# Performance work log

Hardware: AMD Instinct MI355X
Metric: run time of the kernel (lower is better)

## Reference

```python
import jax, jax.numpy as jnp
import numpy as np

K_HARD = 32
K_RAND = 32
SCALE_MAX = 100.0
NEG_FILL = -10000.0
EPS = 1e-12


def _normalize(x):
    return x / jnp.maximum(jnp.linalg.norm(x, axis=1, keepdims=True), EPS)


def _dir_loss(sim, scale, key):
    # One direction of InfoNCE with hard topk negatives + random negatives.
    B = sim.shape[0]
    diag = jnp.eye(B, dtype=bool)
    pos = jnp.diagonal(sim)                       # [B] positives
    sim_neg = jnp.where(diag, NEG_FILL, sim)      # mask self-similarity
    # hard negatives: per-row topk over masked sims (hard_ratio = 1.0)
    hard_vals, hard_idx = jax.lax.top_k(sim_neg, K_HARD)
    # valid pool for random negatives: not diagonal, not already a hard neg
    valid = (~diag).at[jnp.arange(B)[:, None], hard_idx].set(False)
    # uniform sampling without replacement via random-score top_k (fully on-device,
    # replaces the per-row nonzero/randperm loop); B-1-K_HARD >> min_valid_negs here
    r = jnp.where(valid, jax.random.uniform(key, (B, B)), -1.0)
    _, pick = jax.lax.top_k(r, K_RAND)
    rand_vals = jnp.take_along_axis(sim, pick, axis=1)  # picks exclude diag -> sim == sim_neg
    # logits: [pos | hard | rand], target class 0, scaled cross-entropy
    logits = jnp.concatenate([pos[:, None], hard_vals, rand_vals], axis=1) * scale
    return -jnp.mean(jax.nn.log_softmax(logits, axis=1)[:, 0])


def reference(h_img, h_txt, logit_scale):
    a = _normalize(h_img)
    b = _normalize(h_txt)
    sim = a @ b.T                                 # [B, B]
    scale = jnp.minimum(jnp.exp(logit_scale[0]), SCALE_MAX)
    k1, k2 = jax.random.split(jax.random.key(42))
    loss_i2t = _dir_loss(sim, scale, k1)
    loss_t2i = _dir_loss(sim.T, scale, k2)
    return 0.5 * (loss_i2t + loss_t2i)


def setup_inputs() -> dict:
    key = jax.random.key(0)
    k1, k2 = jax.random.split(key)
    B, D = 8192, 1024
    h_img = jax.random.normal(k1, (B, D), dtype=jnp.float32)
    h_txt = jax.random.normal(k2, (B, D), dtype=jnp.float32)
    logit_scale = jnp.full((1,), np.log(1.0 / 0.07), dtype=jnp.float32)
    return {"h_img": h_img, "h_txt": h_txt, "logit_scale": logit_scale}
```

## Files before the change

### kernel.cpp

```cpp
#include <hip/hip_runtime.h>
#include <hip/hip_bf16.h>


#define BN8 8192
#define DK 1024
#define KH 32
#define KR 32
#define LDSZ 131072
#define NCB 128

typedef __attribute__((ext_vector_type(4))) float f32x4;
typedef __attribute__((ext_vector_type(8))) int i32x8;
typedef __attribute__((ext_vector_type(4))) int i32x4;

#if __has_builtin(__builtin_amdgcn_exp2f)
#define EXP2(x) __builtin_amdgcn_exp2f(x)
#else
#define EXP2(x) exp2f(x)
#endif

static __device__ __forceinline__ unsigned short f2bf(float f) {
  unsigned u = __float_as_uint(f);
  u = u + 0x7FFFu + ((u >> 16) & 1u);
  return (unsigned short)(u >> 16);
}
static __device__ __forceinline__ float bf2f(unsigned short v) {
  return __uint_as_float(((unsigned)v) << 16);
}
static __device__ __forceinline__ float keyval(unsigned u) {
  unsigned short v = (u & 0x8000u) ? (unsigned short)(u ^ 0x8000u) : (unsigned short)(~u);
  return bf2f(v);
}

static __device__ __forceinline__ unsigned pk_skey(unsigned w) {
  const unsigned m = ((w >> 15) & 0x00010001u) * 0x7FFFu;
  return w ^ (m | 0x80008000u);
}
static __device__ __forceinline__ unsigned pkmax(unsigned a, unsigned b) {
  unsigned d; asm("v_pk_max_u16 %0, %1, %2" : "=v"(d) : "v"(a), "v"(b)); return d;
}
static __device__ __forceinline__ unsigned pkmin(unsigned a, unsigned b) {
  unsigned d; asm("v_pk_min_u16 %0, %1, %2" : "=v"(d) : "v"(a), "v"(b)); return d;
}
#define INS4P(K0, K1, K2, K3, U) do { unsigned _u = (U); \
    unsigned _n0 = pkmin(K0, _u); K0 = pkmax(K0, _u); \
    unsigned _n1 = pkmin(K1, _n0); K1 = pkmax(K1, _n0); \
    unsigned _n2 = pkmin(K2, _n1); K2 = pkmax(K2, _n1); \
    K3 = pkmax(K3, _n2); } while (0)

__global__ __launch_bounds__(256) void norm_convert8(const float* __restrict__ img,
                                                     const float* __restrict__ txt,
                                                     unsigned char* __restrict__ a8,
                                                     unsigned char* __restrict__ b8) {
  const int row = blockIdx.x;
  const int t = threadIdx.x;
  const float* src;
  unsigned char* dst;
  if (row < BN8) { src = img + (size_t)row * DK; dst = a8 + (size_t)row * DK; }
  else          { src = txt + (size_t)(row - BN8) * DK; dst = b8 + (size_t)(row - BN8) * DK; }
  float4 v = ((const float4*)src)[t];
  float ss = v.x * v.x + v.y * v.y + v.z * v.z + v.w * v.w;
  for (int off = 32; off; off >>= 1) ss += __shfl_xor(ss, off);
  __shared__ float red[4];
  if ((t & 63) == 0) red[t >> 6] = ss;
  __syncthreads();
  float tot = red[0] + red[1] + red[2] + red[3];
  float inv = 1.0f / fmaxf(sqrtf(tot), 1e-12f);
  const int p0 = __builtin_amdgcn_cvt_pk_fp8_f32(v.x * inv, v.y * inv, 0, false);
  const int p1 = __builtin_amdgcn_cvt_pk_fp8_f32(v.z * inv, v.w * inv, 0, false);
  ((unsigned*)dst)[t] = ((unsigned)p0 & 0xFFFFu) | ((unsigned)p1 << 16);
}

#define GLDS(SRC, DST) __builtin_amdgcn_global_load_lds( \
    (const __attribute__((address_space(1))) void*)(SRC), \
    (__attribute__((address_space(3))) void*)(DST), 16, 0, 0)

template <int N> static __device__ __forceinline__ void vmwait() {
  if constexpr (N == 0) asm volatile("s_waitcnt vmcnt(0)" ::: "memory");
  else if constexpr (N == 1) asm volatile("s_waitcnt vmcnt(1)" ::: "memory");
  else if constexpr (N == 2) asm volatile("s_waitcnt vmcnt(2)" ::: "memory");
  else if constexpr (N == 3) asm volatile("s_waitcnt vmcnt(3)" ::: "memory");
  else if constexpr (N == 4) asm volatile("s_waitcnt vmcnt(4)" ::: "memory");
  else if constexpr (N == 5) asm volatile("s_waitcnt vmcnt(5)" ::: "memory");
  else if constexpr (N == 6) asm volatile("s_waitcnt vmcnt(6)" ::: "memory");
}

static __device__ __forceinline__ i32x8 pack8(const char* p0, const char* p1) {
  i32x4 lo = *(const i32x4*)p0;
  i32x4 hi = *(const i32x4*)p1;
  i32x8 r;
  r[0] = lo[0]; r[1] = lo[1]; r[2] = lo[2]; r[3] = lo[3];
  r[4] = hi[0]; r[5] = hi[1]; r[6] = hi[2]; r[7] = hi[3];
  return r;
}

template <int VM, bool STG, int MQ>
static __device__ __forceinline__ void phase8(const char* stg_src, int stg_lds,
                                              char* lds, int cur_off, int kbyte,
                                              int abyte, int bbyte, int sw0, int sw1,
                                              i32x8 (&bfr)[4], f32x4 (&acc)[8][4]) {
  vmwait<VM>();
  asm volatile("s_barrier" ::: "memory");
  const char* cb = lds + cur_off;
  i32x8 af[2];
#pragma unroll
  for (int j = 0; j < 2; ++j)
    af[j] = pack8(cb + abyte + (MQ * 2 + j) * 2048 + sw0,
                  cb + abyte + (MQ * 2 + j) * 2048 + sw1);
  if constexpr (MQ == 0) {
#pragma unroll
    for (int n = 0; n < 4; ++n)
      bfr[n] = pack8(cb + bbyte + n * 2048 + sw0, cb + bbyte + n * 2048 + sw1);
  }
  if constexpr (STG) {
    GLDS(stg_src + kbyte, lds + stg_lds);
    GLDS(stg_src + kbyte + 32768, lds + stg_lds + 4096);
  }
  __builtin_amdgcn_s_setprio(1);
#pragma unroll
  for (int j = 0; j < 2; ++j)
#pragma unroll
    for (int n = 0; n < 4; ++n)
      acc[MQ * 2 + j][n] = __builtin_amdgcn_mfma_scale_f32_16x16x128_f8f6f4(
          af[j], bfr[n], acc[MQ * 2 + j][n], 0, 0,
          0, 0x7F7F7F7F, 0, 0x7F7F7F7F);
  __builtin_amdgcn_s_setprio(0);
}

__global__ __launch_bounds__(512, 2) void gemm_fp8(const unsigned char* __restrict__ A,
                                                   const unsigned char* __restrict__ Bm,
                                                   unsigned short* __restrict__ C) {
  extern __shared__ char lds[];
  const int t = threadIdx.x;
  const int lane = t & 63;
  const int w = t >> 6;
  const int wr = w >> 2, wc = w & 3;
  const int wch = wc >> 1, g4 = wr * 2 + (wc & 1);
  const int llo = lane & 15, lhi = lane >> 4;

  const int bid = blockIdx.y * 32 + blockIdx.x;
  const int swz = (bid & 7) * 128 + (bid >> 3);
  const int row0 = (swz >> 5) << 8;
  const int col0 = (swz & 31) << 8;

  const int scol = (((lane & 7) ^ (lane >> 3)) << 4);
  const char* asg = (const char*)A +
      (size_t)(row0 + wr * 128 + wc * 8 + (lane >> 3)) * 1024 + scol;
  const char* bsg = (const char*)Bm +
      (size_t)(col0 + wch * 128 + g4 * 8 + (lane >> 3)) * 1024 + scol;
  const int ldsAo = wr * 16384 + wc * 1024;
  const int ldsBo = 32768 + wch * 16384 + g4 * 1024;

  const int sw0 = (((2 * lhi) ^ (llo & 7)) << 4);
  const int sw1 = sw0 ^ 16;
  const int abyte = wr * 16384 + llo * 128;
  const int bbyte = 32768 + wc * 8192 + llo * 128;

  f32x4 acc[8][4] = {};
  i32x8 bfr[4];

  {
#pragma unroll
    for (int e = 0; e < 4; ++e) GLDS(bsg + e * 32768, lds + ldsBo + e * 4096);
#pragma unroll
    for (int e = 0; e < 4; ++e) GLDS(asg + e * 32768, lds + ldsAo + e * 4096);
    asm volatile("s_waitcnt vmcnt(0)" ::: "memory");
    asm volatile("s_barrier" ::: "memory");
  }

  for (int u = 0; u < 7; ++u) {
    const int cur = (u & 1) << 16;
    const int nxt = cur ^ 65536;
    const int kb = (u + 1) * 128;
    phase8<3, true, 0>(bsg,         nxt + ldsBo,        lds, cur, kb, abyte, bbyte, sw0, sw1, bfr, acc);
    phase8<4, true, 1>(bsg + 65536, nxt + ldsBo + 8192, lds, cur, kb, abyte, bbyte, sw0, sw1, bfr, acc);
    phase8<5, true, 2>(asg,         nxt + ldsAo,        lds, cur, kb, abyte, bbyte, sw0, sw1, bfr, acc);
    phase8<6, true, 3>(asg + 65536, nxt + ldsAo + 8192, lds, cur, kb, abyte, bbyte, sw0, sw1, bfr, acc);
  }
  {
    const int cur = (7 & 1) << 16;
    phase8<3, false, 0>(asg, 0, lds, cur, 0, abyte, bbyte, sw0, sw1, bfr, acc);
    phase8<2, false, 1>(asg, 0, lds, cur, 0, abyte, bbyte, sw0, sw1, bfr, acc);
    phase8<1, false, 2>(asg, 0, lds, cur, 0, abyte, bbyte, sw0, sw1, bfr, acc);
    phase8<0, false, 3>(asg, 0, lds, cur, 0, abyte, bbyte, sw0, sw1, bfr, acc);
  }

  const int gr0 = row0 + wr * 128 + lhi * 4;
  const int gc0 = col0 + wc * 64 + llo;
#pragma unroll
  for (int m = 0; m < 8; ++m)
#pragma unroll
    for (int n = 0; n < 4; ++n) {
      const int gr = gr0 + m * 16;
      const int gc = gc0 + n * 16;
#pragma unroll
      for (int r = 0; r < 4; ++r)
        C[(size_t)(gr + r) * BN8 + gc] = f2bf(acc[m][n][r]);
    }
}

__global__ __launch_bounds__(512) void fused_reduce(const unsigned short* __restrict__ sim,
                                                    const float* __restrict__ lsc,
                                                    float* __restrict__ losses) {
  __shared__ float sW[8][64];
  __shared__ float hW[8][64];
  __shared__ unsigned mW[8][64];
  __shared__ float posL[64];
  __shared__ unsigned TL[64];
  __shared__ int cnt[18][64];

  const int t = threadIdx.x;
  const int lane = t & 63, w = t >> 6;
  const float s = fminf(__expf(lsc[0]), 100.0f);
  const float s2 = s * 1.44269504f;
  const float c2 = -s2;

  if (blockIdx.x >= NCB) {
    const int i = (blockIdx.x - NCB) * 8 + w;
    const uint4* rowp = (const uint4*)(sim + (size_t)i * BN8);
    uint4 ld[16];
#pragma unroll
    for (int k = 0; k < 16; ++k) ld[k] = rowp[lane + 64 * k];

    const int dlane = (i >> 3) & 63;
    const int dk = i >> 9;
    float pos = 0.f;
    if (lane == dlane) {
      const int wsel = (i >> 1) & 3;
#pragma unroll
      for (int k = 0; k < 16; ++k)
        if (k == dk) {
          unsigned w0;
          if (wsel == 0) w0 = ld[k].x; else if (wsel == 1) w0 = ld[k].y;
          else if (wsel == 2) w0 = ld[k].z; else w0 = ld[k].w;
          pos = bf2f((i & 1) ? (unsigned short)(w0 >> 16) : (unsigned short)(w0 & 0xFFFFu));
          const unsigned nw = (i & 1) ? ((w0 & 0x0000FFFFu) | 0xFF800000u)
                                      : ((w0 & 0xFFFF0000u) | 0x0000FF80u);
          if (wsel == 0) ld[k].x = nw; else if (wsel == 1) ld[k].y = nw;
          else if (wsel == 2) ld[k].z = nw; else ld[k].w = nw;
        }
    }
    pos = __shfl(pos, dlane);

    unsigned k0 = 0, k1 = 0, k2 = 0, k3 = 0;
    float esA = 0.f, esB = 0.f;
#define PWP(W) do { unsigned _w = (W); \
    INS4P(k0, k1, k2, k3, pk_skey(_w)); \
    esA += EXP2(fmaf(__uint_as_float(_w << 16), s2, c2)); \
    esB += EXP2(fmaf(__uint_as_float(_w & 0xFFFF0000u), s2, c2)); } while (0)
#pragma unroll
    for (int k = 0; k < 16; ++k) { PWP(ld[k].x); PWP(ld[k].y); PWP(ld[k].z); PWP(ld[k].w); }
    float es = esA + esB;

    unsigned mk;
    { unsigned a = k0 & 0xFFFFu, b = k0 >> 16; mk = a > b ? a : b; }
    for (int off = 32; off; off >>= 1) { unsigned o = __shfl_xor(mk, off); mk = o > mk ? o : mk; }

#define CNT8(MID) ((int)((k0 & 0xFFFFu) > (MID)) + (int)((k0 >> 16) > (MID)) + \
                   (int)((k1 & 0xFFFFu) > (MID)) + (int)((k1 >> 16) > (MID)) + \
                   (int)((k2 & 0xFFFFu) > (MID)) + (int)((k2 >> 16) > (MID)) + \
                   (int)((k3 & 0xFFFFu) > (MID)) + (int)((k3 >> 16) > (MID)))

    unsigned lo = mk > 576u ? mk - 576u : 0u, hi = mk;
    {
      int c = CNT8(lo);
      for (int off = 32; off; off >>= 1) c += __shfl_xor(c, off);
      if (c < KH) lo = 0;
    }
    while (lo < hi) {
      const unsigned mid = (lo + hi) >> 1;
      int c = CNT8(mid);
      for (int off = 32; off; off >>= 1) c += __shfl_xor(c, off);
      if (c <= KH - 1) hi = mid; else lo = mid + 1;
    }
    const unsigned T = lo;
    int cab = CNT8(T);
    for (int off = 32; off; off >>= 1) cab += __shfl_xor(cab, off);

    float hs = 0.f;
#define HCAND(KK) do { unsigned _a = (KK) & 0xFFFFu, _b = (KK) >> 16; \
    if (_a > T) hs += EXP2(fmaf(keyval(_a), s2, c2)); \
    if (_b > T) hs += EXP2(fmaf(keyval(_b), s2, c2)); } while (0)
    HCAND(k0); HCAND(k1); HCAND(k2); HCAND(k3);
    for (int off = 32; off; off >>= 1) { es += __shfl_xor(es, off); hs += __shfl_xor(hs, off); }

    if (lane == 0) {
      const float hard = hs + (float)(KH - cab) * EXP2(fmaf(keyval(T), s2, c2));
      const float valid = fmaxf(es - hard, 0.f);
      const float rho = (float)KR / (float)(BN8 - 1 - KH);
      const float D = EXP2(fmaf(pos, s2, c2)) + hard + rho * valid;
      losses[i] = s + __logf(D) - s * pos;
    }
    return;
  }

  const int q = t & 7, seg = t >> 3;
  const int c0b = blockIdx.x * 64;

  for (int j = t; j < 18 * 64; j += 512) ((int*)cnt)[j] = 0;

  unsigned kqp[4][4];
  float es[8];
#pragma unroll
  for (int c = 0; c < 4; ++c) {
    es[c * 2] = 0.f; es[c * 2 + 1] = 0.f;
#pragma unroll
    for (int r = 0; r < 4; ++r) kqp[c][r] = 0u;
  }

  const int cq = c0b + q * 8;
  const unsigned short* base = sim + (size_t)(seg * 128) * BN8 + cq;
  for (int rr = 0; rr < 128; rr += 4) {
    uint4 V0 = *(const uint4*)(base + (size_t)(rr + 0) * BN8);
    uint4 V1 = *(const uint4*)(base + (size_t)(rr + 1) * BN8);
    uint4 V2 = *(const uint4*)(base + (size_t)(rr + 2) * BN8);
    uint4 V3 = *(const uint4*)(base + (size_t)(rr + 3) * BN8);
#define COLROW(V, J) do { \
    const unsigned dd = (unsigned)(seg * 128 + rr + (J) - cq); \
    if (dd < 8u) { \
      const int wsel = dd >> 1; \
      unsigned w0; \
      if (wsel == 0) w0 = (V).x; else if (wsel == 1) w0 = (V).y; \
      else if (wsel == 2) w0 = (V).z; else w0 = (V).w; \
      posL[q * 8 + dd] = bf2f((dd & 1) ? (unsigned short)(w0 >> 16) \
                                       : (unsigned short)(w0 & 0xFFFFu)); \
      const unsigned nw = (dd & 1) ? ((w0 & 0x0000FFFFu) | 0xFF800000u) \
                                   : ((w0 & 0xFFFF0000u) | 0x0000FF80u); \
      if (wsel == 0) (V).x = nw; else if (wsel == 1) (V).y = nw; \
      else if (wsel == 2) (V).z = nw; else (V).w = nw; \
    } \
    const unsigned wd0 = (V).x, wd1 = (V).y, wd2 = (V).z, wd3 = (V).w; \
    INS4P(kqp[0][0], kqp[0][1], kqp[0][2], kqp[0][3], pk_skey(wd0)); \
    es[0] += EXP2(fmaf(__uint_as_float(wd0 << 16), s2, c2)); \
    es[1] += EXP2(fmaf(__uint_as_float(wd0 & 0xFFFF0000u), s2, c2)); \
    INS4P(kqp[1][0], kqp[1][1], kqp[1][2], kqp[1][3], pk_skey(wd1)); \
    es[2] += EXP2(fmaf(__uint_as_float(wd1 << 16), s2, c2)); \
    es[3] += EXP2(fmaf(__uint_as_float(wd1 & 0xFFFF0000u), s2, c2)); \
    INS4P(kqp[2][0], kqp[2][1], kqp[2][2], kqp[2][3], pk_skey(wd2)); \
    es[4] += EXP2(fmaf(__uint_as_float(wd2 << 16), s2, c2)); \
    es[5] += EXP2(fmaf(__uint_as_float(wd2 & 0xFFFF0000u), s2, c2)); \
    INS4P(kqp[3][0], kqp[3][1], kqp[3][2], kqp[3][3], pk_skey(wd3)); \
    es[6] += EXP2(fmaf(__uint_as_float(wd3 << 16), s2, c2)); \
    es[7] += EXP2(fmaf(__uint_as_float(wd3 & 0xFFFF0000u), s2, c2)); \
  } while (0)
    COLROW(V0, 0); COLROW(V1, 1); COLROW(V2, 2); COLROW(V3, 3);
  }

  unsigned mk[8];
#pragma unroll
  for (int c = 0; c < 4; ++c) { mk[c * 2] = kqp[c][0] & 0xFFFFu; mk[c * 2 + 1] = kqp[c][0] >> 16; }
#pragma unroll
  for (int d = 8; d <= 32; d <<= 1) {
#pragma unroll
    for (int i = 0; i < 8; ++i) {
      es[i] += __shfl_xor(es[i], d);
      const unsigned om = __shfl_xor(mk[i], d);
      mk[i] = om > mk[i] ? om : mk[i];
    }
  }
  if (lane < 8) {
#pragma unroll
    for (int i = 0; i < 8; ++i) { sW[w][lane * 8 + i] = es[i]; mW[w][lane * 8 + i] = mk[i]; }
  }
  __syncthreads();

  float ETj = 0.f;
  if (t < 64) {
    unsigned mkc = 0;
#pragma unroll
    for (int wv = 0; wv < 8; ++wv) {
      ETj += sW[wv][t];
      mkc = mW[wv][t] > mkc ? mW[wv][t] : mkc;
    }
    mW[0][t] = mkc;
  }
  __syncthreads();

#define CCNT(I, MID) ( \
    (int)((((I) & 1) ? (kqp[(I) >> 1][0] >> 16) : (kqp[(I) >> 1][0] & 0xFFFFu)) > (MID)) + \
    (int)((((I) & 1) ? (kqp[(I) >> 1][1] >> 16) : (kqp[(I) >> 1][1] & 0xFFFFu)) > (MID)) + \
    (int)((((I) & 1) ? (kqp[(I) >> 1][2] >> 16) : (kqp[(I) >> 1][2] & 0xFFFFu)) > (MID)) + \
    (int)((((I) & 1) ? (kqp[(I) >> 1][3] >> 16) : (kqp[(I) >> 1][3] & 0xFFFFu)) > (MID)))

  unsigned lo[8], hi[8];
#pragma unroll
  for (int i = 0; i < 8; ++i) {
    const unsigned m = mW[0][q * 8 + i];
    lo[i] = m > 576u ? m - 576u : 0u;
    hi[i] = m;
    const int cc = CCNT(i, lo[i]);
    if (cc) atomicAdd(&cnt[0][q * 8 + i], cc);
  }
  __syncthreads();
#pragma unroll
  for (int i = 0; i < 8; ++i) if (cnt[0][q * 8 + i] < KH) lo[i] = 0;
  for (int it = 1; it <= 16; ++it) {
#pragma unroll
    for (int i = 0; i < 8; ++i) {
      if (lo[i] < hi[i]) {
        const unsigned mid = (lo[i] + hi[i]) >> 1;
        const int cc = CCNT(i, mid);
        if (cc) atomicAdd(&cnt[it][q * 8 + i], cc);
      }
    }
    __syncthreads();
#pragma unroll
    for (int i = 0; i < 8; ++i) {
      if (lo[i] < hi[i]) {
        const unsigned mid = (lo[i] + hi[i]) >> 1;
        if (cnt[it][q * 8 + i] <= KH - 1) hi[i] = mid; else lo[i] = mid + 1;
      }
    }
  }
#pragma unroll
  for (int i = 0; i < 8; ++i) {
    const int cc = CCNT(i, lo[i]);
    if (cc) atomicAdd(&cnt[17][q * 8 + i], cc);
  }
  if (seg == 0) {
#pragma unroll
    for (int i = 0; i < 8; ++i) TL[q * 8 + i] = lo[i];
  }

  float hs[8];
#pragma unroll
  for (int i = 0; i < 8; ++i) {
    float h = 0.f;
#pragma unroll
    for (int r = 0; r < 4; ++r) {
      const unsigned key = (i & 1) ? (kqp[i >> 1][r] >> 16) : (kqp[i >> 1][r] & 0xFFFFu);
      if (key > lo[i]) h += EXP2(fmaf(keyval(key), s2, c2));
    }
    hs[i] = h;
  }
#pragma unroll
  for (int d = 8; d <= 32; d <<= 1)
#pragma unroll
    for (int i = 0; i < 8; ++i) hs[i] += __shfl_xor(hs[i], d);
  if (lane < 8) {
#pragma unroll
    for (int i = 0; i < 8; ++i) hW[w][lane * 8 + i] = hs[i];
  }
  __syncthreads();

  if (t < 64) {
    float hard = 0.f;
#pragma unroll
    for (int wv = 0; wv < 8; ++wv) hard += hW[wv][t];
    const int cab = cnt[17][t];
    const unsigned T = TL[t];
    hard += (float)(KH - cab) * EXP2(fmaf(keyval(T), s2, c2));
    const float posj = posL[t];
    const float valid = fmaxf(ETj - hard, 0.f);
    const float rho = (float)KR / (float)(BN8 - 1 - KH);
    const float D = EXP2(fmaf(posj, s2, c2)) + hard + rho * valid;
    losses[BN8 + c0b + t] = s + __logf(D) - s * posj;
  }
}

__global__ __launch_bounds__(256) void finalize(const float* __restrict__ losses,
                                                float* __restrict__ out) {
  float ssum = 0.f;
  for (int j = threadIdx.x; j < 2 * BN8; j += 256) ssum += losses[j];
  for (int off = 32; off; off >>= 1) ssum += __shfl_xor(ssum, off);
  __shared__ float red[4];
  if ((threadIdx.x & 63) == 0) red[threadIdx.x >> 6] = ssum;
  __syncthreads();
  if (threadIdx.x == 0)
    out[0] = (red[0] + red[1] + red[2] + red[3]) / (2.0f * BN8);
}

extern "C" void kernel_launch(void* const* d_in, const int* in_sizes, int n_in,
                              void* d_out, int out_size, void* d_ws, size_t ws_size,
                              hipStream_t stream) {
  const float* img = (const float*)d_in[0];
  const float* txt = (const float*)d_in[1];
  const float* lsc = (const float*)d_in[2];
  float* out = (float*)d_out;
  char* ws = (char*)d_ws;

  unsigned char* a8 = (unsigned char*)ws;
  unsigned char* b8 = (unsigned char*)(ws + (8u << 20));
  float* losses = (float*)(ws + (16u << 20));
  unsigned short* simb = (unsigned short*)(ws + (16u << 20) + (1u << 16));

  norm_convert8<<<2 * BN8, 256, 0, stream>>>(img, txt, a8, b8);

  gemm_fp8<<<dim3(32, 32), 512, LDSZ, stream>>>(a8, b8, simb);
  fused_reduce<<<NCB + 1024, 512, 0, stream>>>(simb, lsc, losses);

  finalize<<<1, 256, 0, stream>>>(losses, out);
}
```

Baseline: 191.5 us.

## Replace four-phase staged GEMM pipeline with one barrier per k-step double buffer

```diff
diff --git a/kernel.cpp b/kernel.cpp
--- a/kernel.cpp
+++ b/kernel.cpp
@@ -75,16 +75,6 @@
     (const __attribute__((address_space(1))) void*)(SRC), \
     (__attribute__((address_space(3))) void*)(DST), 16, 0, 0)
 
-template <int N> static __device__ __forceinline__ void vmwait() {
-  if constexpr (N == 0) asm volatile("s_waitcnt vmcnt(0)" ::: "memory");
-  else if constexpr (N == 1) asm volatile("s_waitcnt vmcnt(1)" ::: "memory");
-  else if constexpr (N == 2) asm volatile("s_waitcnt vmcnt(2)" ::: "memory");
-  else if constexpr (N == 3) asm volatile("s_waitcnt vmcnt(3)" ::: "memory");
-  else if constexpr (N == 4) asm volatile("s_waitcnt vmcnt(4)" ::: "memory");
-  else if constexpr (N == 5) asm volatile("s_waitcnt vmcnt(5)" ::: "memory");
-  else if constexpr (N == 6) asm volatile("s_waitcnt vmcnt(6)" ::: "memory");
-}
-
 static __device__ __forceinline__ i32x8 pack8(const char* p0, const char* p1) {
   i32x4 lo = *(const i32x4*)p0;
   i32x4 hi = *(const i32x4*)p1;
@@ -92,39 +82,6 @@
   r[0] = lo[0]; r[1] = lo[1]; r[2] = lo[2]; r[3] = lo[3];
   r[4] = hi[0]; r[5] = hi[1]; r[6] = hi[2]; r[7] = hi[3];
   return r;
-}
-
-template <int VM, bool STG, int MQ>
-static __device__ __forceinline__ void phase8(const char* stg_src, int stg_lds,
-                                              char* lds, int cur_off, int kbyte,
-                                              int abyte, int bbyte, int sw0, int sw1,
-                                              i32x8 (&bfr)[4], f32x4 (&acc)[8][4]) {
-  vmwait<VM>();
-  asm volatile("s_barrier" ::: "memory");
-  const char* cb = lds + cur_off;
-  i32x8 af[2];
-#pragma unroll
-  for (int j = 0; j < 2; ++j)
-    af[j] = pack8(cb + abyte + (MQ * 2 + j) * 2048 + sw0,
-                  cb + abyte + (MQ * 2 + j) * 2048 + sw1);
-  if constexpr (MQ == 0) {
-#pragma unroll
-    for (int n = 0; n < 4; ++n)
-      bfr[n] = pack8(cb + bbyte + n * 2048 + sw0, cb + bbyte + n * 2048 + sw1);
-  }
-  if constexpr (STG) {
-    GLDS(stg_src + kbyte, lds + stg_lds);
-    GLDS(stg_src + kbyte + 32768, lds + stg_lds + 4096);
-  }
-  __builtin_amdgcn_s_setprio(1);
-#pragma unroll
-  for (int j = 0; j < 2; ++j)
-#pragma unroll
-    for (int n = 0; n < 4; ++n)
-      acc[MQ * 2 + j][n] = __builtin_amdgcn_mfma_scale_f32_16x16x128_f8f6f4(
-          af[j], bfr[n], acc[MQ * 2 + j][n], 0, 0,
-          0, 0x7F7F7F7F, 0, 0x7F7F7F7F);
-  __builtin_amdgcn_s_setprio(0);
 }
 
 __global__ __launch_bounds__(512, 2) void gemm_fp8(const unsigned char* __restrict__ A,
@@ -157,7 +114,6 @@
   const int bbyte = 32768 + wc * 8192 + llo * 128;
 
   f32x4 acc[8][4] = {};
-  i32x8 bfr[4];
 
   {
 #pragma unroll
@@ -165,24 +121,42 @@
 #pragma unroll
     for (int e = 0; e < 4; ++e) GLDS(asg + e * 32768, lds + ldsAo + e * 4096);
     asm volatile("s_waitcnt vmcnt(0)" ::: "memory");
+  }
+
+  for (int u = 0; u < 8; ++u) {
     asm volatile("s_barrier" ::: "memory");
-  }
-
-  for (int u = 0; u < 7; ++u) {
     const int cur = (u & 1) << 16;
     const int nxt = cur ^ 65536;
-    const int kb = (u + 1) * 128;
-    phase8<3, true, 0>(bsg,         nxt + ldsBo,        lds, cur, kb, abyte, bbyte, sw0, sw1, bfr, acc);
-    phase8<4, true, 1>(bsg + 65536, nxt + ldsBo + 8192, lds, cur, kb, abyte, bbyte, sw0, sw1, bfr, acc);
-    phase8<5, true, 2>(asg,         nxt + ldsAo,        lds, cur, kb, abyte, bbyte, sw0, sw1, bfr, acc);
-    phase8<6, true, 3>(asg + 65536, nxt + ldsAo + 8192, lds, cur, kb, abyte, bbyte, sw0, sw1, bfr, acc);
-  }
-  {
-    const int cur = (7 & 1) << 16;
-    phase8<3, false, 0>(asg, 0, lds, cur, 0, abyte, bbyte, sw0, sw1, bfr, acc);
-    phase8<2, false, 1>(asg, 0, lds, cur, 0, abyte, bbyte, sw0, sw1, bfr, acc);
-    phase8<1, false, 2>(asg, 0, lds, cur, 0, abyte, bbyte, sw0, sw1, bfr, acc);
-    phase8<0, false, 3>(asg, 0, lds, cur, 0, abyte, bbyte, sw0, sw1, bfr, acc);
+    if (u < 7) {
+      const int kb = (u + 1) * 128;
+#pragma unroll
+      for (int e = 0; e < 4; ++e) GLDS(bsg + e * 32768 + kb, lds + nxt + ldsBo + e * 4096);
+#pragma unroll
+      for (int e = 0; e < 4; ++e) GLDS(asg + e * 32768 + kb, lds + nxt + ldsAo + e * 4096);
+    }
+    const char* cb = lds + cur;
+    i32x8 bfr[4];
+#pragma unroll
+    for (int n = 0; n < 4; ++n)
+      bfr[n] = pack8(cb + bbyte + n * 2048 + sw0, cb + bbyte + n * 2048 + sw1);
+#pragma unroll
+    for (int MQ = 0; MQ < 4; ++MQ) {
+      i32x8 af[2];
+#pragma unroll
+      for (int j = 0; j < 2; ++j)
+        af[j] = pack8(cb + abyte + (MQ * 2 + j) * 2048 + sw0,
+                      cb + abyte + (MQ * 2 + j) * 2048 + sw1);
+      __builtin_amdgcn_s_setprio(1);
+#pragma unroll
+      for (int j = 0; j < 2; ++j)
+#pragma unroll
+        for (int n = 0; n < 4; ++n)
+          acc[MQ * 2 + j][n] = __builtin_amdgcn_mfma_scale_f32_16x16x128_f8f6f4(
+              af[j], bfr[n], acc[MQ * 2 + j][n], 0, 0,
+              0, 0x7F7F7F7F, 0, 0x7F7F7F7F);
+      __builtin_amdgcn_s_setprio(0);
+    }
+    if (u < 7) asm volatile("s_waitcnt vmcnt(0)" ::: "memory");
   }
 
   const int gr0 = row0 + wr * 128 + lhi * 4;
```

New measurement: 191.7 us. No clear change (+0.1%).
